# Kernel optimization log

Measured on AMD Instinct MI355X. Metric: run time of the kernel, lower is better.

## Reference

```python
import jax, jax.numpy as jnp
import numpy as np

TAU = 1.5
LAM = 0.9
BATCH_SIZE = 32
E = float(np.e)


def _bce(p, t):
    # torch BCELoss(reduction='none'): -(t*log(p) + (1-t)*log(1-p)), logs clamped at -100
    log_p = jnp.clip(jnp.log(p), -100.0)
    log_1p = jnp.clip(jnp.log1p(-p), -100.0)
    return -(t * log_p + (1.0 - t) * log_1p)


def _lambertw(y, iters=12):
    # Principal-branch Lambert W for y >= -1/e, via Halley's method.
    # Init: series near the branch point for y<0, log1p elsewhere.
    w = jnp.where(
        y < 0.0,
        -1.0 + jnp.sqrt(jnp.maximum(2.0 * (1.0 + E * y), 0.0)),
        jnp.log1p(y),
    )
    eps = 1e-12
    for _ in range(iters):
        ew = jnp.exp(w)
        f = w * ew - y
        denom = ew * (w + 1.0) - (w + 2.0) * f / (2.0 * (w + 1.0) + eps)
        w = w - f / (denom + eps)
    return w


def setup_inputs() -> dict:
    key = jax.random.key(0)
    k1, k2 = jax.random.split(key)
    shape = (16, 2048, 1024)
    logits = jax.random.uniform(k1, shape, jnp.float32, 1e-6, 1.0 - 1e-6)
    targets = jax.random.uniform(k2, shape, jnp.float32)
    return {"logits": logits, "targets": targets}


def reference(logits, targets):
    l = _bce(logits, targets)
    l_det = jax.lax.stop_gradient(l)
    # y = 0.5 * max(-2/e, (l_i - tau)/lam)  >= -1/e
    y = 0.5 * jnp.maximum(-2.0 / E, (l_det - TAU) / LAM)
    w = _lambertw(y)          # log(sigma) = -W(y)
    sigma = jnp.exp(-w)       # sigma = exp(-W(y)), constant w.r.t. grads
    loss = (l - TAU) * sigma + LAM * w * w
    return loss.sum() / BATCH_SIZE
```

## Files before the change

kernel.cpp:

```cpp
#include <hip/hip_runtime.h>


#define TAU_F      1.5f
#define LAM_F      0.9f
#define INV_LAM_F  1.1111111111111112f
#define E_F        2.718281828459045f
#define NEG_2_E_F  -0.7357588823428847f
#define LOG2E_F    1.4426950408889634f
#define LN2_F      0.6931471805599453f

__device__ __forceinline__ float fexp(float x) {
    return __builtin_amdgcn_exp2f(x * LOG2E_F);
}
__device__ __forceinline__ float flog(float x) {
    return __builtin_amdgcn_logf(x) * LN2_F;
}
__device__ __forceinline__ float frcp(float x) {
    return __builtin_amdgcn_rcpf(x);
}

__device__ __forceinline__ float superloss_elem(float p, float t) {
    float log_p  = fmaxf(flog(p), -100.0f);
    float log_1p = fmaxf(flog(1.0f - p), -100.0f);
    float l  = -(t * log_p + (1.0f - t) * log_1p);
    float lt = l - TAU_F;
    float y  = 0.5f * fmaxf(NEG_2_E_F, lt * INV_LAM_F);

    float s  = __builtin_amdgcn_sqrtf(fmaxf(2.0f * fmaf(E_F, y, 1.0f), 0.0f));
    float w  = (y < 0.0f) ? (s - 1.0f) : flog(1.0f + y);

    #pragma unroll
    for (int i = 0; i < 4; ++i) {
        float ew    = fexp(w);
        float f     = fmaf(w, ew, -y);
        float wp1   = w + 1.0f;
        float a     = 2.0f * wp1 + 1e-12f;
        float denom = ew * wp1 - (w + 2.0f) * f * frcp(a);
        w = w - f * frcp(denom + 1e-12f);
    }

    float sigma = fexp(-w);
    return fmaf(lt, sigma, LAM_F * w * w);
}

__global__ __launch_bounds__(256) void superloss_kernel(
        const float4* __restrict__ p4, const float4* __restrict__ t4,
        float* __restrict__ out, int n4, int n_tail, const float* __restrict__ p_s,
        const float* __restrict__ t_s) {
    int idx    = blockIdx.x * blockDim.x + threadIdx.x;
    int stride = gridDim.x * blockDim.x;
    float acc = 0.0f;
    for (int i = idx; i < n4; i += stride) {
        float4 p = p4[i];
        float4 t = t4[i];
        acc += superloss_elem(p.x, t.x);
        acc += superloss_elem(p.y, t.y);
        acc += superloss_elem(p.z, t.z);
        acc += superloss_elem(p.w, t.w);
    }
    if (idx == 0) {
        for (int i = 4 * n4; i < 4 * n4 + n_tail; ++i)
            acc += superloss_elem(p_s[i], t_s[i]);
    }

    #pragma unroll
    for (int off = 32; off > 0; off >>= 1)
        acc += __shfl_down(acc, off, 64);

    __shared__ float wsum[4];
    int lane = threadIdx.x & 63;
    int wid  = threadIdx.x >> 6;
    if (lane == 0) wsum[wid] = acc;
    __syncthreads();
    if (threadIdx.x == 0) {
        float s = (wsum[0] + wsum[1]) + (wsum[2] + wsum[3]);
        atomicAdd(out, s * (1.0f / 32.0f));
    }
}

extern "C" void kernel_launch(void* const* d_in, const int* in_sizes, int n_in,
                              void* d_out, int out_size, void* d_ws, size_t ws_size,
                              hipStream_t stream) {
    const float* logits  = (const float*)d_in[0];
    const float* targets = (const float*)d_in[1];
    float* out = (float*)d_out;
    int n  = in_sizes[0];
    int n4 = n / 4;
    int n_tail = n - 4 * n4;

    hipMemsetAsync(d_out, 0, sizeof(float), stream);

    const int block = 256;
    const int grid  = 2048;
    superloss_kernel<<<grid, block, 0, stream>>>(
        (const float4*)logits, (const float4*)targets, out, n4, n_tail,
        logits, targets);
}
```

Before: 283.6 us.

## Simplify Lambert-W superloss algebra and cut Halley iterations with better init

Rewrites the per-element math: the BCE is computed with one fewer multiply in log2 domain, the branch-point initial guess uses a third-order series, and Halley's update is restructured to need a single reciprocal per iteration. It halves the Halley iteration count and removes the final exp by using the identity sigma = W/y, so the loss becomes lam*w*(w+2), with a closed-form value for the clamped branch. This targets the transcendental/ALU cost of a compute-bound elementwise kernel. It drops the -100 log clamps and fewer iterations may reduce accuracy for some inputs.

```diff
diff --git a/kernel.cpp b/kernel.cpp
--- a/kernel.cpp
+++ b/kernel.cpp
@@ -1,46 +1,46 @@
 #include <hip/hip_runtime.h>
 
 
-#define TAU_F      1.5f
-#define LAM_F      0.9f
-#define INV_LAM_F  1.1111111111111112f
-#define E_F        2.718281828459045f
-#define NEG_2_E_F  -0.7357588823428847f
-#define LOG2E_F    1.4426950408889634f
-#define LN2_F      0.6931471805599453f
+#define TAU_F       1.5f
+#define LAM_F       0.9f
+#define E_F         2.718281828459045f
+#define NEG_INV_E_F -0.36787944117144233f
+#define INV_2LAM_F  0.5555555555555556f
+#define LOG2E_F     1.4426950408889634f
+#define LN2_F       0.6931471805599453f
 
-__device__ __forceinline__ float fexp(float x) {
-    return __builtin_amdgcn_exp2f(x * LOG2E_F);
-}
-__device__ __forceinline__ float flog(float x) {
-    return __builtin_amdgcn_logf(x) * LN2_F;
-}
-__device__ __forceinline__ float frcp(float x) {
-    return __builtin_amdgcn_rcpf(x);
-}
+__device__ __forceinline__ float fexp2(float x) { return __builtin_amdgcn_exp2f(x); }
+__device__ __forceinline__ float flog2(float x) { return __builtin_amdgcn_logf(x); }
+__device__ __forceinline__ float frcp(float x)  { return __builtin_amdgcn_rcpf(x); }
+__device__ __forceinline__ float fsqrt(float x) { return __builtin_amdgcn_sqrtf(x); }
 
 __device__ __forceinline__ float superloss_elem(float p, float t) {
-    float log_p  = fmaxf(flog(p), -100.0f);
-    float log_1p = fmaxf(flog(1.0f - p), -100.0f);
-    float l  = -(t * log_p + (1.0f - t) * log_1p);
-    float lt = l - TAU_F;
-    float y  = 0.5f * fmaxf(NEG_2_E_F, lt * INV_LAM_F);
+    float lgp  = flog2(p);
+    float lg1p = flog2(1.0f - p);
+    float l    = -LN2_F * fmaf(t, lgp - lg1p, lg1p);
+    float lt   = l - TAU_F;
+    float y    = lt * INV_2LAM_F;
+    bool  clamped = (y < NEG_INV_E_F);
+    float yc   = fmaxf(y, NEG_INV_E_F);
 
-    float s  = __builtin_amdgcn_sqrtf(fmaxf(2.0f * fmaf(E_F, y, 1.0f), 0.0f));
-    float w  = (y < 0.0f) ? (s - 1.0f) : flog(1.0f + y);
+    float s     = fsqrt(fmaxf(fmaf(2.0f * E_F, yc, 2.0f), 0.0f));
+    float w_neg = fmaf(s, fmaf(s, fmaf(s, 11.0f / 72.0f, -1.0f / 3.0f), 1.0f), -1.0f);
+    float w_pos = LN2_F * flog2(1.0f + yc);
+    float w     = (yc < 0.0f) ? w_neg : w_pos;
 
     #pragma unroll
-    for (int i = 0; i < 4; ++i) {
-        float ew    = fexp(w);
-        float f     = fmaf(w, ew, -y);
-        float wp1   = w + 1.0f;
-        float a     = 2.0f * wp1 + 1e-12f;
-        float denom = ew * wp1 - (w + 2.0f) * f * frcp(a);
-        w = w - f * frcp(denom + 1e-12f);
+    for (int i = 0; i < 2; ++i) {
+        float ew   = fexp2(w * LOG2E_F);
+        float f    = fmaf(w, ew, -yc);
+        float wp1  = w + 1.0f;
+        float num  = 2.0f * f * wp1;
+        float den  = fmaf(2.0f * ew, wp1 * wp1, -(w + 2.0f) * f) + 1e-12f;
+        w = w - num * frcp(den);
     }
 
-    float sigma = fexp(-w);
-    return fmaf(lt, sigma, LAM_F * w * w);
+    float loss_un = LAM_F * (w * (w + 2.0f));
+    float loss_cl = fmaf(lt, E_F, LAM_F);
+    return clamped ? loss_cl : loss_un;
 }
 
 __global__ __launch_bounds__(256) void superloss_kernel(
@@ -73,8 +73,8 @@
     if (lane == 0) wsum[wid] = acc;
     __syncthreads();
     if (threadIdx.x == 0) {
-        float s = (wsum[0] + wsum[1]) + (wsum[2] + wsum[3]);
-        atomicAdd(out, s * (1.0f / 32.0f));
+        float sblk = (wsum[0] + wsum[1]) + (wsum[2] + wsum[3]);
+        atomicAdd(out, sblk * (1.0f / 32.0f));
     }
 }
 
```

New measurement: 283.9 us. No clear change (+0.1%).
